# Optimization experiments

Measured on AMD Instinct MI355X. Metric: run time of the kernel, lower is better.

The kernel has to match this reference:

```python
import jax, jax.numpy as jnp
import numpy as np

N, E, D, H, HID = 50000, 400000, 64, 8, 1024
NEG_SLOPE = 0.2
BN_EPS = 1e-5


def setup_inputs() -> dict:
    key = jax.random.key(0)
    ks = jax.random.split(key, 10)
    s = 0.05
    return {
        "x": jax.random.normal(ks[0], (N, D), jnp.float32),
        "src": jax.random.randint(ks[1], (E,), 0, N, jnp.int32),
        "dst": jax.random.randint(ks[2], (E,), 0, N, jnp.int32),
        "fc_w": jax.random.normal(ks[3], (H * D, D), jnp.float32) * s,
        "attn_l": jax.random.normal(ks[4], (H, D), jnp.float32) * s,
        "attn_r": jax.random.normal(ks[5], (H, D), jnp.float32) * s,
        "gat_bias": jnp.zeros((H * D,), jnp.float32),
        "bn1_gamma": jnp.ones((H * D,), jnp.float32),
        "bn1_beta": jnp.zeros((H * D,), jnp.float32),
        "w1": jax.random.normal(ks[6], (HID, H * D), jnp.float32) * s,
        "b1": jnp.zeros((HID,), jnp.float32),
        "w2": jax.random.normal(ks[7], (D, HID), jnp.float32) * s,
        "b2": jnp.zeros((D,), jnp.float32),
        "bn2_gamma": jnp.ones((D,), jnp.float32),
        "bn2_beta": jnp.zeros((D,), jnp.float32),
    }


def _batchnorm(h, gamma, beta):
    # training-mode BatchNorm1d: batch statistics over node axis
    mu = h.mean(axis=0)
    var = h.var(axis=0)
    return gamma * (h - mu) * jax.lax.rsqrt(var + BN_EPS) + beta


def reference(x, src, dst, fc_w, attn_l, attn_r, gat_bias,
              bn1_gamma, bn1_beta, w1, b1, w2, b2, bn2_gamma, bn2_beta):
    n = x.shape[0]
    nh, dh = attn_l.shape
    # --- GATConv ---
    feat = (x @ fc_w.T).reshape(n, nh, dh)                 # [N,H,Dh]
    el = jnp.einsum("nhd,hd->nh", feat, attn_l)            # [N,H]
    er = jnp.einsum("nhd,hd->nh", feat, attn_r)            # [N,H]
    e = jax.nn.leaky_relu(el[src] + er[dst], NEG_SLOPE)    # [E,H]
    # edge softmax grouped by destination node (numerically stable)
    emax = jax.ops.segment_max(e, dst, num_segments=n)
    emax = jnp.where(jnp.isfinite(emax), emax, 0.0)        # nodes w/ no in-edges
    ez = jnp.exp(e - emax[dst])
    denom = jax.ops.segment_sum(ez, dst, num_segments=n)
    alpha = ez / denom[dst]                                # [E,H]
    msg = alpha[:, :, None] * feat[src]                    # [E,H,Dh]
    rst = jax.ops.segment_sum(msg, dst, num_segments=n)    # [N,H,Dh]
    rst = rst + gat_bias.reshape(nh, dh)
    h = rst.reshape(n, nh * dh)                            # flatten(1)
    # --- feed forward: BN -> Linear -> ReLU -> Linear -> BN ---
    h = _batchnorm(h, bn1_gamma, bn1_beta)
    h = jax.nn.relu(h @ w1.T + b1)
    h = h @ w2.T + b2
    h = _batchnorm(h, bn2_gamma, bn2_beta)
    return h
```

## Files before the change

kernel.cpp:

```cpp
#include <hip/hip_runtime.h>

#define NEG_SLOPE 0.2f
#define BN_EPS 1e-5f

typedef __bf16 bf16x8 __attribute__((ext_vector_type(8)));
typedef float  f32x4  __attribute__((ext_vector_type(4)));
typedef unsigned short ushort8_t __attribute__((ext_vector_type(8)));

__device__ __forceinline__ unsigned short f2bf(float f) {
    unsigned int u = __float_as_uint(f);
    unsigned int r = u + 0x7FFFu + ((u >> 16) & 1u);
    return (unsigned short)(r >> 16);
}
__device__ __forceinline__ float bf2f(unsigned short u) {
    return __uint_as_float(((unsigned int)u) << 16);
}
__device__ __forceinline__ void gload16(const void* g, void* l) {
    __builtin_amdgcn_global_load_lds(
        (const __attribute__((address_space(1))) unsigned int*)g,
        (__attribute__((address_space(3))) unsigned int*)l, 16, 0, 0);
}

__global__ __launch_bounds__(256)
void prep(const float* __restrict__ x, const int* __restrict__ dst,
          const float* __restrict__ fc_w, const float* __restrict__ w2,
          const float* __restrict__ attn_l, const float* __restrict__ attn_r,
          const float* __restrict__ b2,
          unsigned short* __restrict__ xbf, unsigned short* __restrict__ fcwbf,
          unsigned short* __restrict__ w2bf, float* __restrict__ proj,
          int* __restrict__ counts, float* __restrict__ outp,
          int totX4, int E, int totO4,
          int bCvtx, int bHist, int bFcw, int bW2, int bOut)
{
    const int bid = blockIdx.x, tid = threadIdx.x;
    if (bid < bCvtx) {
        int i4 = bid * 256 + tid;
        if (i4 < totX4) {
            float4 v = *(const float4*)(x + (size_t)i4 * 4);
            ushort4 o = {f2bf(v.x), f2bf(v.y), f2bf(v.z), f2bf(v.w)};
            *(ushort4*)(xbf + (size_t)i4 * 4) = o;
        }
    } else if (bid < bHist) {
        int base = (bid - bCvtx) * 1024 + tid;
        #pragma unroll
        for (int k = 0; k < 4; ++k) {
            int e = base + k * 256;
            if (e < E) atomicAdd(&counts[dst[e]], 1);
        }
    } else if (bid < bFcw) {
        int i4 = (bid - bHist) * 256 + tid;
        if (i4 < 8192) {
            float4 v = *(const float4*)(fc_w + (size_t)i4 * 4);
            ushort4 o = {f2bf(v.x), f2bf(v.y), f2bf(v.z), f2bf(v.w)};
            *(ushort4*)(fcwbf + (size_t)i4 * 4) = o;
        }
    } else if (bid < bW2) {
        int i4 = (bid - bFcw) * 256 + tid;
        if (i4 < 16384) {
            float4 v = *(const float4*)(w2 + (size_t)i4 * 4);
            ushort4 o = {f2bf(v.x), f2bf(v.y), f2bf(v.z), f2bf(v.w)};
            *(ushort4*)(w2bf + (size_t)i4 * 4) = o;
        }
    } else if (bid < bOut) {
        int i4 = (bid - bW2) * 256 + tid;
        if (i4 < totO4) {
            float4 v = *(const float4*)(b2 + (i4 & 15) * 4);
            *(float4*)(outp + (size_t)i4 * 4) = v;
        }
    } else {
        for (int t2 = tid; t2 < 512; t2 += 256) {
            int h = t2 >> 6, k = t2 & 63;
            float al = 0.f, ar = 0.f;
            for (int d = 0; d < 64; ++d) {
                float w = fc_w[(size_t)(h * 64 + d) * 64 + k];
                al = fmaf(attn_l[h * 64 + d], w, al);
                ar = fmaf(attn_r[h * 64 + d], w, ar);
            }
            proj[t2] = al;
            proj[512 + t2] = ar;
        }
    }
}

__global__ __launch_bounds__(256)
void scan1_elr(const int* __restrict__ counts, int* __restrict__ incl,
               int* __restrict__ bsum, int N, int NB,
               const float* __restrict__ x, const float* __restrict__ proj,
               float* __restrict__ el, float* __restrict__ er, int NH)
{
    __shared__ int sm[256];
    if ((int)blockIdx.x < NB) {
        int i = blockIdx.x * 256 + threadIdx.x;
        int v = (i < N) ? counts[i] : 0;
        sm[threadIdx.x] = v;
        __syncthreads();
        #pragma unroll
        for (int d = 1; d < 256; d <<= 1) {
            int t = (threadIdx.x >= d) ? sm[threadIdx.x - d] : 0;
            __syncthreads();
            sm[threadIdx.x] += t;
            __syncthreads();
        }
        if (i < N) incl[i] = sm[threadIdx.x];
        if (threadIdx.x == 255) bsum[blockIdx.x] = sm[255];
    } else {
        int idx = (blockIdx.x - NB) * 256 + threadIdx.x;
        if (idx >= NH) return;
        int h = idx & 7, n = idx >> 3;
        const float4* f  = (const float4*)(x + (size_t)n * 64);
        const float4* pl = (const float4*)(proj + h * 64);
        const float4* pr = (const float4*)(proj + 512 + h * 64);
        float sl = 0.f, sr = 0.f;
        #pragma unroll
        for (int i = 0; i < 16; ++i) {
            float4 fv = f[i], lv = pl[i], rv = pr[i];
            sl += fv.x * lv.x + fv.y * lv.y + fv.z * lv.z + fv.w * lv.w;
            sr += fv.x * rv.x + fv.y * rv.y + fv.z * rv.z + fv.w * rv.w;
        }
        el[idx] = sl;
        er[idx] = sr;
    }
}

__global__ void scan23(const int* __restrict__ incl, const int* __restrict__ bsum,
                       int* __restrict__ row_ptr, int* __restrict__ cursor, int N, int NB)
{
    __shared__ int sm[256];
    int t = threadIdx.x;
    sm[t] = (t < (int)blockIdx.x && t < NB) ? bsum[t] : 0;
    __syncthreads();
    #pragma unroll
    for (int d = 128; d > 0; d >>= 1) {
        if (t < d) sm[t] += sm[t + d];
        __syncthreads();
    }
    int pre = sm[0];
    int i = blockIdx.x * 256 + t;
    if (i < N) {
        int v = incl[i] + pre;
        row_ptr[i + 1] = v;
        cursor[i + 1] = v;
    }
    if (i == 0) { row_ptr[0] = 0; cursor[0] = 0; }
}

__global__ void scatter_edges(const int* __restrict__ src, const int* __restrict__ dst,
                              int* __restrict__ cursor, int* __restrict__ esrc, int E) {
    int e = blockIdx.x * 256 + threadIdx.x;
    if (e < E) {
        int p = atomicAdd(&cursor[dst[e]], 1);
        esrc[p] = src[e];
    }
}

__global__ __launch_bounds__(256)
void gat_aggregate(const int* __restrict__ row_ptr, const int* __restrict__ esrc,
                   const float* __restrict__ el, const float* __restrict__ er,
                   const unsigned short* __restrict__ xb, unsigned short* __restrict__ xagg,
                   int N)
{
    int node = blockIdx.x * 4 + (threadIdx.x >> 6);
    if (node >= N) return;
    const int lane = threadIdx.x & 63;
    const int h = lane >> 3, j = lane & 7;
    const int beg = row_ptr[node], end = row_ptr[node + 1];
    const float er_n = er[node * 8 + h];

    float denom = 0.f;
    float a[8] = {};
    int s_cur = (beg < end) ? esrc[beg] : 0;
    for (int k = beg; k < end; ++k) {
        int s_nxt = (k + 1 < end) ? esrc[k + 1] : 0;
        float elv = el[s_cur * 8 + h];
        ushort8_t fv = *(const ushort8_t*)(xb + (size_t)s_cur * 64 + j * 8);
        float v = elv + er_n;
        v = (v > 0.f) ? v : NEG_SLOPE * v;
        float z = __expf(v);
        denom += z;
        #pragma unroll
        for (int t = 0; t < 8; ++t) a[t] = fmaf(z, bf2f(fv[t]), a[t]);
        s_cur = s_nxt;
    }
    float inv = (end > beg) ? 1.f / denom : 0.f;
    ushort8_t o;
    #pragma unroll
    for (int t = 0; t < 8; ++t) o[t] = f2bf(a[t] * inv);
    *(ushort8_t*)(xagg + (size_t)node * 512 + lane * 8) = o;
}

__global__ __launch_bounds__(256)
void bn1_stats(const unsigned short* __restrict__ Xa,
               const unsigned short* __restrict__ Fw,
               const float* __restrict__ gat_bias,
               float* __restrict__ sums1, int M)
{
    __shared__ alignas(16) char Asm[128 * 64 * 2];
    __shared__ alignas(16) char Bsm[64 * 64 * 2];
    __shared__ float reds[4][64], redq[4][64];
    const int tid = threadIdx.x, lane = tid & 63, wave = tid >> 6;
    const int bm = blockIdx.x * 128;
    const int head = blockIdx.y;
    const int lr = lane >> 3, lk = ((lane & 7) ^ lr) * 8;

    #pragma unroll
    for (int it = 0; it < 4; ++it) {
        int seg = wave * 4 + it;
        gload16(Xa + (size_t)(bm + seg * 8 + lr) * 512 + head * 64 + lk, Asm + seg * 1024);
    }
    #pragma unroll
    for (int it = 0; it < 2; ++it) {
        int seg = wave * 2 + it;
        gload16(Fw + (size_t)(head * 64 + seg * 8 + lr) * 64 + lk, Bsm + seg * 1024);
    }
    __syncthreads();

    f32x4 acc[2][4] = {};
    #pragma unroll
    for (int kk = 0; kk < 2; ++kk) {
        int kg = kk * 4 + (lane >> 4);
        bf16x8 a[2], b[4];
        #pragma unroll
        for (int i = 0; i < 2; ++i) {
            int row = wave * 32 + i * 16 + (lane & 15);
            a[i] = *(const bf16x8*)(Asm + row * 128 + ((kg ^ (row & 7)) << 4));
        }
        #pragma unroll
        for (int j = 0; j < 4; ++j) {
            int row = j * 16 + (lane & 15);
            b[j] = *(const bf16x8*)(Bsm + row * 128 + ((kg ^ (row & 7)) << 4));
        }
        #pragma unroll
        for (int i = 0; i < 2; ++i)
            #pragma unroll
            for (int j = 0; j < 4; ++j)
                acc[i][j] = __builtin_amdgcn_mfma_f32_16x16x32_bf16(a[i], b[j], acc[i][j], 0, 0, 0);
    }

    float s4[4] = {}, q4[4] = {};
    #pragma unroll
    for (int j = 0; j < 4; ++j) {
        int col = j * 16 + (lane & 15);
        float bias = gat_bias[head * 64 + col];
        #pragma unroll
        for (int i = 0; i < 2; ++i)
            #pragma unroll
            for (int r = 0; r < 4; ++r) {
                int gm = bm + wave * 32 + i * 16 + (lane >> 4) * 4 + r;
                if (gm < M) {
                    float vq = bf2f(f2bf(acc[i][j][r] + bias));
                    s4[j] += vq; q4[j] += vq * vq;
                }
            }
    }
    #pragma unroll
    for (int j = 0; j < 4; ++j) {
        s4[j] += __shfl_xor(s4[j], 16); q4[j] += __shfl_xor(q4[j], 16);
        s4[j] += __shfl_xor(s4[j], 32); q4[j] += __shfl_xor(q4[j], 32);
    }
    if (lane < 16) {
        #pragma unroll
        for (int j = 0; j < 4; ++j) {
            reds[wave][j * 16 + lane] = s4[j];
            redq[wave][j * 16 + lane] = q4[j];
        }
    }
    __syncthreads();
    if (wave == 0 && lane < 16) {
        #pragma unroll
        for (int j = 0; j < 4; ++j) {
            int c = j * 16 + lane;
            atomicAdd(&sums1[head * 64 + c], reds[0][c] + reds[1][c] + reds[2][c] + reds[3][c]);
            atomicAdd(&sums1[512 + head * 64 + c], redq[0][c] + redq[1][c] + redq[2][c] + redq[3][c]);
        }
    }
}

__global__ __launch_bounds__(256)
void fold(const float* __restrict__ w1, const float* __restrict__ fc_w,
          const float* __restrict__ sums1, const float* __restrict__ gamma,
          const float* __restrict__ beta, const float* __restrict__ gat_bias,
          const float* __restrict__ b1, unsigned short* __restrict__ wtil,
          float* __restrict__ b1p, float invM)
{
    const int bid = blockIdx.x, tid = threadIdx.x;
    if (bid < 64) {
        __shared__ float sF[64][65];
        __shared__ float sa[64];
        int ot = bid >> 3, h = bid & 7;
        if (tid < 64) {
            int c = h * 64 + tid;
            float mu = sums1[c] * invM;
            float var = sums1[512 + c] * invM - mu * mu;
            sa[tid] = gamma[c] * rsqrtf(var + BN_EPS);
        }
        for (int e = 0; e < 16; ++e) {
            int idx = tid * 16 + e;
            int d = idx >> 6, k = idx & 63;
            sF[k][d] = fc_w[(size_t)(h * 64 + d) * 64 + k];
        }
        __syncthreads();
        int ol = tid >> 1, half = tid & 1;
        int o = ot * 128 + ol;
        int kbase = half * 32;
        float acc[32];
        #pragma unroll
        for (int i = 0; i < 32; ++i) acc[i] = 0.f;
        const float* wrow = w1 + (size_t)o * 512 + h * 64;
        #pragma unroll
        for (int dc = 0; dc < 4; ++dc) {
            float wa[16];
            #pragma unroll
            for (int d = 0; d < 16; ++d) wa[d] = wrow[dc * 16 + d] * sa[dc * 16 + d];
            #pragma unroll
            for (int kk2 = 0; kk2 < 32; ++kk2) {
                float s = acc[kk2];
                #pragma unroll
                for (int d = 0; d < 16; ++d) s = fmaf(wa[d], sF[kbase + kk2][dc * 16 + d], s);
                acc[kk2] = s;
            }
        }
        unsigned int* orow = (unsigned int*)(wtil + (size_t)o * 512 + h * 64 + kbase);
        #pragma unroll
        for (int i = 0; i < 16; ++i)
            orow[i] = (unsigned int)f2bf(acc[2 * i]) | ((unsigned int)f2bf(acc[2 * i + 1]) << 16);
    } else {
        __shared__ float ss[512];
        for (int c = tid; c < 512; c += 256) {
            float mu = sums1[c] * invM;
            float var = sums1[512 + c] * invM - mu * mu;
            float a = gamma[c] * rsqrtf(var + BN_EPS);
            ss[c] = beta[c] + a * (gat_bias[c] - mu);
        }
        __syncthreads();
        int wave = tid >> 6, lane = tid & 63;
        int o = (bid - 64) * 4 + wave;
        const float* wrow = w1 + (size_t)o * 512 + lane * 8;
        float p = 0.f;
        #pragma unroll
        for (int t2 = 0; t2 < 8; ++t2) p = fmaf(wrow[t2], ss[lane * 8 + t2], p);
        #pragma unroll
        for (int d = 1; d < 64; d <<= 1) p += __shfl_xor(p, d);
        if (lane == 0) b1p[o] = b1[o] + p;
    }
}

__global__ __launch_bounds__(256)
void gemm2p(const unsigned short* __restrict__ A,
            const unsigned short* __restrict__ B,
            const unsigned short* __restrict__ W2,
            const float* __restrict__ b1p,
            float* __restrict__ outp,
            int M)
{
    __shared__ alignas(16) char smem[49152];
    char* Abuf0 = smem;
    char* Abuf1 = smem + 16384;
    char* Bbuf  = smem + 32768;
    char* TR   = smem;
    char* Wbuf = smem + 32768;

    const int tid = threadIdx.x, lane = tid & 63, wave = tid >> 6;
    const int wr = wave >> 1, wc = wave & 1;
    const int lr = lane >> 3, lk = ((lane & 7) ^ lr) * 8;

    int bid = blockIdx.x;
    int wgid = (bid & 7) * 391 + (bid >> 3);
    const int bm = (wgid >> 3) * 128;
    const int t  = wgid & 7;
    const int bn = t * 128;

    #pragma unroll
    for (int it = 0; it < 4; ++it) {
        int seg = wave * 4 + it;
        gload16(A + (size_t)(bm + seg * 8 + lr) * 512 + lk, Abuf0 + seg * 1024);
    }

    f32x4 acc[4][4] = {};
    #pragma unroll
    for (int ks = 0; ks < 8; ++ks) {
        const int k0 = ks * 64;
        #pragma unroll
        for (int it = 0; it < 4; ++it) {
            int seg = wave * 4 + it;
            gload16(B + (size_t)(bn + seg * 8 + lr) * 512 + k0 + lk, Bbuf + seg * 1024);
        }
        if (ks < 7) {
            char* An = (ks & 1) ? Abuf0 : Abuf1;
            #pragma unroll
            for (int it = 0; it < 4; ++it) {
                int seg = wave * 4 + it;
                gload16(A + (size_t)(bm + seg * 8 + lr) * 512 + (k0 + 64) + lk, An + seg * 1024);
            }
            asm volatile("s_waitcnt vmcnt(4)" ::: "memory");
        } else {
            asm volatile("s_waitcnt vmcnt(0)" ::: "memory");
        }
        __builtin_amdgcn_s_barrier();
        __builtin_amdgcn_sched_barrier(0);
        const char* Ac = (ks & 1) ? Abuf1 : Abuf0;
        #pragma unroll
        for (int kk = 0; kk < 2; ++kk) {
            int kg = kk * 4 + (lane >> 4);
            bf16x8 a[4], b[4];
            #pragma unroll
            for (int i = 0; i < 4; ++i) {
                int row = wr * 64 + i * 16 + (lane & 15);
                a[i] = *(const bf16x8*)(Ac + row * 128 + ((kg ^ (row & 7)) << 4));
            }
            #pragma unroll
            for (int j = 0; j < 4; ++j) {
                int row = wc * 64 + j * 16 + (lane & 15);
                b[j] = *(const bf16x8*)(Bbuf + row * 128 + ((kg ^ (row & 7)) << 4));
            }
            #pragma unroll
            for (int i = 0; i < 4; ++i)
                #pragma unroll
                for (int j = 0; j < 4; ++j)
                    acc[i][j] = __builtin_amdgcn_mfma_f32_16x16x32_bf16(a[i], b[j], acc[i][j], 0, 0, 0);
        }
        __builtin_amdgcn_sched_barrier(0);
        __builtin_amdgcn_s_barrier();
        __builtin_amdgcn_sched_barrier(0);
    }

    #pragma unroll
    for (int j = 0; j < 4; ++j) {
        int c = wc * 64 + j * 16 + (lane & 15);
        float bs = b1p[bn + c];
        #pragma unroll
        for (int i = 0; i < 4; ++i)
            #pragma unroll
            for (int r = 0; r < 4; ++r) {
                int rw = wr * 64 + i * 16 + (lane >> 4) * 4 + r;
                float v = fmaxf(acc[i][j][r] + bs, 0.f);
                *(unsigned short*)(TR + rw * 256 + (((c >> 3) ^ (rw & 7)) << 4) + (c & 7) * 2) = f2bf(v);
            }
    }
    #pragma unroll
    for (int it = 0; it < 4; ++it) {
        int oc = wave * 16 + it * 4 + (lane >> 4);
        int g = lane & 15;
        gload16(W2 + (size_t)oc * 1024 + bn + ((g ^ (oc & 7))) * 8, Wbuf + (wave * 4 + it) * 1024);
    }
    __syncthreads();

    f32x4 pacc[2][4] = {};
    #pragma unroll
    for (int ks = 0; ks < 4; ++ks) {
        int kg2 = ks * 4 + (lane >> 4);
        #pragma unroll
        for (int i = 0; i < 2; ++i) {
            int arow = wave * 32 + i * 16 + (lane & 15);
            bf16x8 av = *(const bf16x8*)(TR + arow * 256 + ((kg2 ^ (arow & 7)) << 4));
            #pragma unroll
            for (int j = 0; j < 4; ++j) {
                int oc = j * 16 + (lane & 15);
                bf16x8 bv = *(const bf16x8*)(Wbuf + oc * 256 + ((kg2 ^ (oc & 7)) << 4));
                pacc[i][j] = __builtin_amdgcn_mfma_f32_16x16x32_bf16(av, bv, pacc[i][j], 0, 0, 0);
            }
        }
    }

    #pragma unroll
    for (int i = 0; i < 2; ++i)
        #pragma unroll
        for (int j = 0; j < 4; ++j)
            #pragma unroll
            for (int r = 0; r < 4; ++r) {
                int gm = bm + wave * 32 + i * 16 + (lane >> 4) * 4 + r;
                int col = j * 16 + (lane & 15);
                if (gm < M) atomicAdd(&outp[(size_t)gm * 64 + col], pacc[i][j][r]);
            }
}

__global__ __launch_bounds__(256)
void bn2_stats(const float* __restrict__ outp, int M, float* __restrict__ sums2)
{
    __shared__ float ls[256], lq[256];
    int c = threadIdx.x & 63, g = threadIdx.x >> 6;
    float s = 0.f, q = 0.f;
    for (int r = blockIdx.x * 4 + g; r < M; r += gridDim.x * 4) {
        float v = outp[(size_t)r * 64 + c];
        s += v; q += v * v;
    }
    ls[threadIdx.x] = s; lq[threadIdx.x] = q;
    __syncthreads();
    if (g == 0) {
        s = ls[c] + ls[64 + c] + ls[128 + c] + ls[192 + c];
        q = lq[c] + lq[64 + c] + lq[128 + c] + lq[192 + c];
        atomicAdd(&sums2[c], s);
        atomicAdd(&sums2[64 + c], q);
    }
}

__global__ __launch_bounds__(256)
void bn_apply64(float* __restrict__ X, const float* __restrict__ sums2,
                const float* __restrict__ gamma, const float* __restrict__ beta,
                int M, float invM)
{
    int c = threadIdx.x & 63, g = threadIdx.x >> 6;
    float mu = sums2[c] * invM;
    float var = sums2[64 + c] * invM - mu * mu;
    float a = gamma[c] * rsqrtf(var + BN_EPS);
    float b = beta[c] - a * mu;
    for (int r = blockIdx.x * 4 + g; r < M; r += gridDim.x * 4) {
        size_t i = (size_t)r * 64 + c;
        X[i] = fmaf(a, X[i], b);
    }
}

extern "C" void kernel_launch(void* const* d_in, const int* in_sizes, int n_in,
                              void* d_out, int out_size, void* d_ws, size_t ws_size,
                              hipStream_t stream)
{
    const float* x         = (const float*)d_in[0];
    const int*   src       = (const int*)d_in[1];
    const int*   dst       = (const int*)d_in[2];
    const float* fc_w      = (const float*)d_in[3];
    const float* attn_l    = (const float*)d_in[4];
    const float* attn_r    = (const float*)d_in[5];
    const float* gat_bias  = (const float*)d_in[6];
    const float* bn1_gamma = (const float*)d_in[7];
    const float* bn1_beta  = (const float*)d_in[8];
    const float* w1        = (const float*)d_in[9];
    const float* b1        = (const float*)d_in[10];
    const float* w2        = (const float*)d_in[11];
    const float* b2        = (const float*)d_in[12];
    const float* bn2_gamma = (const float*)d_in[13];
    const float* bn2_beta  = (const float*)d_in[14];
    float* out = (float*)d_out;

    const int D = 64, HD = 512, HID = 1024;
    const int N = in_sizes[0] / D;
    const int E = in_sizes[1];
    const int NH = N * 8;
    const int NB = (N + 255) / 256;
    const int Mpad = ((N + 127) / 128) * 128 + 128;

    size_t off = 0;
    auto alloc = [&](size_t bytes) -> void* {
        void* p = (char*)d_ws + off;
        off += (bytes + 255) & ~(size_t)255;
        return p;
    };
    unsigned short* xagg = (unsigned short*)alloc((size_t)Mpad * HD * 2);
    unsigned short* xbf  = (unsigned short*)alloc((size_t)N * D * 2);
    unsigned short* fcwbf = (unsigned short*)alloc((size_t)HD * D * 2);
    unsigned short* wtil = (unsigned short*)alloc((size_t)HID * HD * 2);
    unsigned short* w2bf = (unsigned short*)alloc((size_t)D * HID * 2);
    float* b1p   = (float*)alloc(HID * 4);
    float* proj  = (float*)alloc(2 * 512 * 4);
    float* el    = (float*)alloc((size_t)NH * 4);
    float* er    = (float*)alloc((size_t)NH * 4);
    char* zbase  = (char*)d_ws + off;
    int* counts  = (int*)alloc((size_t)N * 4);
    float* sums1 = (float*)alloc(2 * 512 * 4);
    float* sums2 = (float*)alloc(2 * 64 * 4);
    size_t zbytes = ((char*)d_ws + off) - zbase;
    int* incl    = (int*)alloc((size_t)N * 4);
    int* row_ptr = (int*)alloc((size_t)(N + 1) * 4);
    int* cursor  = (int*)alloc((size_t)(N + 1) * 4);
    int* bsum    = (int*)alloc(256 * 4);
    int* esrc    = (int*)alloc((size_t)E * 4);
    (void)ws_size; (void)n_in; (void)out_size;

    hipMemsetAsync(zbase, 0, zbytes, stream);

    {
        int totX4 = (N * D) / 4;
        int totO4 = (N * D) / 4;
        int bCvtx = (totX4 + 255) / 256;
        int bHist = bCvtx + (E + 1023) / 1024;
        int bFcw  = bHist + 32;
        int bW2   = bFcw + 64;
        int bOut  = bW2 + (totO4 + 255) / 256;
        int grid  = bOut + 1;
        prep<<<grid, 256, 0, stream>>>(x, dst, fc_w, w2, attn_l, attn_r, b2,
                                       xbf, fcwbf, w2bf, proj, counts, out,
                                       totX4, E, totO4, bCvtx, bHist, bFcw, bW2, bOut);
    }

    scan1_elr<<<NB + (NH + 255) / 256, 256, 0, stream>>>(counts, incl, bsum, N, NB,
                                                         x, proj, el, er, NH);
    scan23<<<NB, 256, 0, stream>>>(incl, bsum, row_ptr, cursor, N, NB);
    scatter_edges<<<(E + 255) / 256, 256, 0, stream>>>(src, dst, cursor, esrc, E);

    gat_aggregate<<<(N + 3) / 4, 256, 0, stream>>>(row_ptr, esrc, el, er, xbf, xagg, N);

    {
        dim3 grid((N + 127) / 128, 8);
        bn1_stats<<<grid, 256, 0, stream>>>(xagg, fcwbf, gat_bias, sums1, N);
    }
    fold<<<320, 256, 0, stream>>>(w1, fc_w, sums1, bn1_gamma, bn1_beta, gat_bias,
                                  b1, wtil, b1p, 1.f / N);

    {
        int nwg = ((N + 127) / 128) * 8;
        gemm2p<<<nwg, 256, 0, stream>>>(xagg, wtil, w2bf, b1p, out, N);
    }

    bn2_stats<<<1024, 256, 0, stream>>>(out, N, sums2);
    bn_apply64<<<1024, 256, 0, stream>>>(out, sums2, bn2_gamma, bn2_beta, N, 1.f / N);
}
```

Measured before the change: 332.4 us.

## Replace gemm2 split-K float atomics with bf16 partial buffers reduced in BN2 stats

The second GEMM's per-column-tile partial outputs are no longer atomically added into the fp32 output. Each tile is staged through LDS and written as bf16 into one of 8 partial buffers, and the BN2 stats kernel sums them with the bias and writes the output. This also drops the bias pre-fill from prep. It removes heavy global atomic traffic in exchange for extra partial-buffer writes and reads, and it adds bf16 rounding error to the partial sums.

```diff
diff --git a/kernel.cpp b/kernel.cpp
--- a/kernel.cpp
+++ b/kernel.cpp
@@ -25,12 +25,10 @@
 void prep(const float* __restrict__ x, const int* __restrict__ dst,
           const float* __restrict__ fc_w, const float* __restrict__ w2,
           const float* __restrict__ attn_l, const float* __restrict__ attn_r,
-          const float* __restrict__ b2,
           unsigned short* __restrict__ xbf, unsigned short* __restrict__ fcwbf,
           unsigned short* __restrict__ w2bf, float* __restrict__ proj,
-          int* __restrict__ counts, float* __restrict__ outp,
-          int totX4, int E, int totO4,
-          int bCvtx, int bHist, int bFcw, int bW2, int bOut)
+          int* __restrict__ counts, int totX4, int E,
+          int bCvtx, int bHist, int bFcw, int bW2)
 {
     const int bid = blockIdx.x, tid = threadIdx.x;
     if (bid < bCvtx) {
@@ -60,12 +58,6 @@
             float4 v = *(const float4*)(w2 + (size_t)i4 * 4);
             ushort4 o = {f2bf(v.x), f2bf(v.y), f2bf(v.z), f2bf(v.w)};
             *(ushort4*)(w2bf + (size_t)i4 * 4) = o;
-        }
-    } else if (bid < bOut) {
-        int i4 = (bid - bW2) * 256 + tid;
-        if (i4 < totO4) {
-            float4 v = *(const float4*)(b2 + (i4 & 15) * 4);
-            *(float4*)(outp + (size_t)i4 * 4) = v;
         }
     } else {
         for (int t2 = tid; t2 < 512; t2 += 256) {
@@ -349,7 +341,7 @@
             const unsigned short* __restrict__ B,
             const unsigned short* __restrict__ W2,
             const float* __restrict__ b1p,
-            float* __restrict__ outp,
+            unsigned short* __restrict__ P,
             int M)
 {
     __shared__ alignas(16) char smem[49152];
@@ -358,6 +350,7 @@
     char* Bbuf  = smem + 32768;
     char* TR   = smem;
     char* Wbuf = smem + 32768;
+    char* PK   = smem + 32768;
 
     const int tid = threadIdx.x, lane = tid & 63, wave = tid >> 6;
     const int wr = wave >> 1, wc = wave & 1;
@@ -460,6 +453,7 @@
             }
         }
     }
+    __syncthreads();
 
     #pragma unroll
     for (int i = 0; i < 2; ++i)
@@ -467,20 +461,39 @@
         for (int j = 0; j < 4; ++j)
             #pragma unroll
             for (int r = 0; r < 4; ++r) {
-                int gm = bm + wave * 32 + i * 16 + (lane >> 4) * 4 + r;
+                int row = wave * 32 + i * 16 + (lane >> 4) * 4 + r;
                 int col = j * 16 + (lane & 15);
-                if (gm < M) atomicAdd(&outp[(size_t)gm * 64 + col], pacc[i][j][r]);
-            }
-}
-
-__global__ __launch_bounds__(256)
-void bn2_stats(const float* __restrict__ outp, int M, float* __restrict__ sums2)
+                *(unsigned short*)(PK + row * 128 + col * 2) = f2bf(pacc[i][j][r]);
+            }
+    __syncthreads();
+    unsigned short* Pt = P + (size_t)t * M * 64;
+    #pragma unroll
+    for (int it = 0; it < 4; ++it) {
+        int u = it * 256 + tid;
+        int row = u >> 3, g8 = u & 7;
+        int gm = bm + row;
+        if (gm < M) {
+            uint4 v = *(const uint4*)(PK + row * 128 + g8 * 16);
+            *(uint4*)(Pt + (size_t)gm * 64 + g8 * 8) = v;
+        }
+    }
+}
+
+__global__ __launch_bounds__(256)
+void reduce_bn2(const unsigned short* __restrict__ P, const float* __restrict__ b2,
+                float* __restrict__ out, int M, float* __restrict__ sums2)
 {
     __shared__ float ls[256], lq[256];
     int c = threadIdx.x & 63, g = threadIdx.x >> 6;
+    const size_t S = (size_t)M * 64;
+    float bias = b2[c];
     float s = 0.f, q = 0.f;
     for (int r = blockIdx.x * 4 + g; r < M; r += gridDim.x * 4) {
-        float v = outp[(size_t)r * 64 + c];
+        size_t idx = (size_t)r * 64 + c;
+        float v = bias;
+        #pragma unroll
+        for (int t = 0; t < 8; ++t) v += bf2f(P[t * S + idx]);
+        out[idx] = v;
         s += v; q += v * v;
     }
     ls[threadIdx.x] = s; lq[threadIdx.x] = q;
@@ -544,6 +557,7 @@
         return p;
     };
     unsigned short* xagg = (unsigned short*)alloc((size_t)Mpad * HD * 2);
+    unsigned short* P    = (unsigned short*)alloc((size_t)8 * N * D * 2);
     unsigned short* xbf  = (unsigned short*)alloc((size_t)N * D * 2);
     unsigned short* fcwbf = (unsigned short*)alloc((size_t)HD * D * 2);
     unsigned short* wtil = (unsigned short*)alloc((size_t)HID * HD * 2);
@@ -568,16 +582,14 @@
 
     {
         int totX4 = (N * D) / 4;
-        int totO4 = (N * D) / 4;
         int bCvtx = (totX4 + 255) / 256;
         int bHist = bCvtx + (E + 1023) / 1024;
         int bFcw  = bHist + 32;
         int bW2   = bFcw + 64;
-        int bOut  = bW2 + (totO4 + 255) / 256;
-        int grid  = bOut + 1;
-        prep<<<grid, 256, 0, stream>>>(x, dst, fc_w, w2, attn_l, attn_r, b2,
-                                       xbf, fcwbf, w2bf, proj, counts, out,
-                                       totX4, E, totO4, bCvtx, bHist, bFcw, bW2, bOut);
+        int grid  = bW2 + 1;
+        prep<<<grid, 256, 0, stream>>>(x, dst, fc_w, w2, attn_l, attn_r,
+                                       xbf, fcwbf, w2bf, proj, counts,
+                                       totX4, E, bCvtx, bHist, bFcw, bW2);
     }
 
     scan1_elr<<<NB + (NH + 255) / 256, 256, 0, stream>>>(counts, incl, bsum, N, NB,
@@ -596,9 +608,9 @@
 
     {
         int nwg = ((N + 127) / 128) * 8;
-        gemm2p<<<nwg, 256, 0, stream>>>(xagg, wtil, w2bf, b1p, out, N);
-    }
-
-    bn2_stats<<<1024, 256, 0, stream>>>(out, N, sums2);
+        gemm2p<<<nwg, 256, 0, stream>>>(xagg, wtil, w2bf, b1p, P, N);
+    }
+
+    reduce_bn2<<<1024, 256, 0, stream>>>(P, b2, out, N, sums2);
     bn_apply64<<<1024, 256, 0, stream>>>(out, sums2, bn2_gamma, bn2_beta, N, 1.f / N);
 }
```

Measured after the change: 294.5 us. -11.4%, faster.
